# Kernel optimization log

Measured on AMD Instinct MI355X. Metric: run time of the kernel, lower is better.

## Reference

```python
import jax, jax.numpy as jnp
import numpy as np

B, S, E, H = 2, 2048, 768, 12
DK = E // H


def setup_inputs() -> dict:
    key = jax.random.key(0)
    ks = jax.random.split(key, 8)
    scale = 1.0 / np.sqrt(E)
    return {
        "key": jax.random.normal(ks[0], (B, S, E), jnp.float32),
        "query": jax.random.normal(ks[1], (B, S, E), jnp.float32),
        "value": jax.random.normal(ks[2], (B, S, E), jnp.float32),
        "mask": jax.random.randint(ks[3], (1, 1, S, S), 0, 2, jnp.int32),
        # nn.Linear params (w_k used for q/k/v as in the source; w_o output proj)
        "Wk": jax.random.uniform(ks[4], (E, E), jnp.float32, -scale, scale),
        "bk": jax.random.uniform(ks[5], (E,), jnp.float32, -scale, scale),
        "Wo": jax.random.uniform(ks[6], (E, E), jnp.float32, -scale, scale),
        "bo": jax.random.uniform(ks[7], (E,), jnp.float32, -scale, scale),
    }


def reference(key, query, value, mask, Wk, bk, Wo, bo):
    # NOTE: source module (faithfully) projects q, k, v all with w_k.
    k = (key @ Wk.T + bk).reshape(B, S, H, DK).transpose(0, 2, 1, 3)    # [B,H,S,DK]
    q = (query @ Wk.T + bk).reshape(B, S, H, DK).transpose(0, 2, 1, 3)
    v = (value @ Wk.T + bk).reshape(B, S, H, DK).transpose(0, 2, 1, 3)
    # quirk: scores MULTIPLIED by sqrt(d_k) (source bug, preserved)
    scores = jnp.einsum("bhsd,bhtd->bhst", q, k) * jnp.sqrt(jnp.float32(DK))
    # quirk: masked positions set to 1e-6 (not -inf), BEFORE softmax
    scores = jnp.where(mask == 0, jnp.float32(1e-6), scores)
    # dropout=0.0 -> identity (applied pre-softmax in source)
    attn = jax.nn.softmax(scores, axis=-1)                               # [B,H,S,S]
    x = jnp.einsum("bhst,bhtd->bhsd", attn, v)                           # [B,H,S,DK]
    x = x.transpose(0, 2, 1, 3).reshape(B, S, E)
    return x @ Wo.T + bo
```

## Files before the change

kernel.cpp:

```cpp
#include <hip/hip_runtime.h>

#define BB 2
#define SS 2048
#define EE 768
#define HH 12
#define DKK 64

typedef _Float16 h16;
typedef _Float16 half8 __attribute__((ext_vector_type(8)));
typedef _Float16 h16x4 __attribute__((ext_vector_type(4)));
typedef float f32x4 __attribute__((ext_vector_type(4)));

__global__ void pack_mask_k(const int* __restrict__ mask, unsigned* __restrict__ mp) {
    int idx = blockIdx.x * 256 + threadIdx.x;
    int base = idx * 32;
    const int4* m4 = (const int4*)(mask + base);
    unsigned w = 0;
#pragma unroll
    for (int i = 0; i < 8; ++i) {
        int4 v = m4[i];
        if (v.x) w |= 1u << (i * 4 + 0);
        if (v.y) w |= 1u << (i * 4 + 1);
        if (v.z) w |= 1u << (i * 4 + 2);
        if (v.w) w |= 1u << (i * 4 + 3);
    }
    mp[idx] = w;
}

__launch_bounds__(256)
__global__ void proj_gemm_k(const float* __restrict__ srcK, const float* __restrict__ srcQ,
                            const float* __restrict__ srcV, const float* __restrict__ Wk,
                            const float* __restrict__ bk,
                            h16* __restrict__ kh, h16* __restrict__ qh, h16* __restrict__ vtp) {
    __shared__ h16 As[64 * 64];
    __shared__ h16 Bs[128 * 64];
    const int bid = blockIdx.x;
    const int idx = (bid & 7) * 144 + (bid >> 3);
    const int z = idx / 384;
    const int rem = idx % 384;
    const int m0 = (rem / 6) * 64, n0 = (rem % 6) * 128;
    const float* src = (z == 0) ? srcK : ((z == 1) ? srcQ : srcV);
    const int tid = threadIdx.x, lane = tid & 63, wid = tid >> 6;
    const int l = lane & 15, gq = lane >> 4;
    f32x4 acc[4][2] = {};

    for (int k0 = 0; k0 < EE; k0 += 64) {
#pragma unroll
        for (int it = 0; it < 2; ++it) {
            int e8 = it * 256 + tid;
            int row = e8 >> 3, g = e8 & 7;
            const float* pa = src + (m0 + row) * EE + k0 + g * 8;
            float4 a0 = *(const float4*)pa, a1 = *(const float4*)(pa + 4);
            half8 ha = {(h16)a0.x, (h16)a0.y, (h16)a0.z, (h16)a0.w,
                        (h16)a1.x, (h16)a1.y, (h16)a1.z, (h16)a1.w};
            *(half8*)((char*)As + row * 128 + ((g ^ (row & 7)) << 4)) = ha;
        }
#pragma unroll
        for (int it = 0; it < 4; ++it) {
            int e8 = it * 256 + tid;
            int row = e8 >> 3, g = e8 & 7;
            const float* pb = Wk + (n0 + row) * EE + k0 + g * 8;
            float4 b0 = *(const float4*)pb, b1 = *(const float4*)(pb + 4);
            half8 hb = {(h16)b0.x, (h16)b0.y, (h16)b0.z, (h16)b0.w,
                        (h16)b1.x, (h16)b1.y, (h16)b1.z, (h16)b1.w};
            *(half8*)((char*)Bs + row * 128 + ((g ^ (row & 7)) << 4)) = hb;
        }
        __syncthreads();
#pragma unroll
        for (int ks = 0; ks < 2; ++ks) {
            half8 a[4], b[2];
#pragma unroll
            for (int rf = 0; rf < 4; ++rf) {
                int row = rf * 16 + l;
                int g = (ks * 4 + gq) ^ (row & 7);
                a[rf] = *(const half8*)((const char*)As + row * 128 + (g << 4));
            }
#pragma unroll
            for (int cf = 0; cf < 2; ++cf) {
                int row = wid * 32 + cf * 16 + l;
                int g = (ks * 4 + gq) ^ (row & 7);
                b[cf] = *(const half8*)((const char*)Bs + row * 128 + (g << 4));
            }
            __builtin_amdgcn_s_setprio(1);
#pragma unroll
            for (int rf = 0; rf < 4; ++rf)
#pragma unroll
                for (int cf = 0; cf < 2; ++cf)
                    acc[rf][cf] = __builtin_amdgcn_mfma_f32_16x16x32_f16(a[rf], b[cf], acc[rf][cf], 0, 0, 0);
            __builtin_amdgcn_s_setprio(0);
        }
        __syncthreads();
    }
    if (z == 2) {
#pragma unroll
        for (int rf = 0; rf < 4; ++rf)
#pragma unroll
            for (int cf = 0; cf < 2; ++cf) {
                int n = n0 + wid * 32 + cf * 16 + l;
                float bias = bk[n];
                int h = n >> 6, d = n & 63;
                int mb = m0 + rf * 16 + gq * 4;
                int b = mb >> 11, s = mb & 2047;
                h16x4 pv = {(h16)(acc[rf][cf][0] + bias), (h16)(acc[rf][cf][1] + bias),
                            (h16)(acc[rf][cf][2] + bias), (h16)(acc[rf][cf][3] + bias)};
                *(h16x4*)(vtp + ((long)((b * HH + h) * 64 + d)) * SS + s) = pv;
            }
    } else {
        h16* dst = (z == 0) ? kh : qh;
#pragma unroll
        for (int rf = 0; rf < 4; ++rf)
#pragma unroll
            for (int cf = 0; cf < 2; ++cf) {
                int n = n0 + wid * 32 + cf * 16 + l;
                float bias = bk[n];
                int h = n >> 6, d = n & 63;
#pragma unroll
                for (int j = 0; j < 4; ++j) {
                    int m = m0 + rf * 16 + gq * 4 + j;
                    int b = m >> 11, s = m & 2047;
                    dst[(((long)(b * HH + h) * SS + s) << 6) + d] = (h16)(acc[rf][cf][j] + bias);
                }
            }
    }
}

struct StageRegs { half8 k[2], v[2]; };

__device__ __forceinline__ void ld_stage(StageRegs& r, const h16* __restrict__ kg,
                                         const h16* __restrict__ vg,
                                         int kv0, int wid, int lane) {
    int rr = lane >> 3;
    int sg = (lane & 7) ^ rr;
#pragma unroll
    for (int i = 0; i < 2; ++i) {
        int row = wid * 16 + i * 8 + rr;
        r.k[i] = *(const half8*)(kg + (long)(kv0 + row) * DKK + sg * 8);
        r.v[i] = *(const half8*)(vg + (long)row * SS + kv0 + sg * 8);
    }
}

__device__ __forceinline__ void st_stage(h16* __restrict__ kl, h16* __restrict__ vl,
                                         const StageRegs& r, int wid, int lane) {
#pragma unroll
    for (int i = 0; i < 2; ++i) {
        *(half8*)(kl + wid * 1024 + i * 512 + lane * 8) = r.k[i];
        *(half8*)(vl + wid * 1024 + i * 512 + lane * 8) = r.v[i];
    }
}

__launch_bounds__(256, 3)
__global__ void attn_k(const h16* __restrict__ qh, const h16* __restrict__ kh,
                       const h16* __restrict__ vt, const unsigned long long* __restrict__ mp,
                       h16* __restrict__ xh) {
    __shared__ h16 Kbuf[2][4096];
    __shared__ h16 Vbuf[2][4096];
    __shared__ char Ps[8192];
    const int tid = threadIdx.x;
    const int lane = tid & 63, wid = tid >> 6;
    const int l = lane & 15, g = lane >> 4;
    const int bid = blockIdx.x;
    const int idx = (bid & 7) * 96 + (bid >> 3);
    const int q0 = (idx & 31) * 64 + wid * 16;
    const int bh = idx >> 5;
    const long base = (long)bh * SS * DKK;
    const h16* kg = kh + base;
    const h16* vg = vt + base;
    char* pbase = Ps + wid * 2048;

    half8 qf0, qf1;
    {
        const h16* qp = qh + base + (long)(q0 + l) * DKK + g * 8;
        qf0 = *(const half8*)qp;
        qf1 = *(const half8*)(qp + 32);
    }
    const unsigned long long* mrow = mp + (long)(q0 + l) * (SS / 64);

    f32x4 o[4] = {};
    float m2 = -INFINITY, lsum = 0.f;
    const float K2 = 8.0f * 1.44269504f;
    const float C2 = 1e-6f * 1.44269504f;

    StageRegs sr;
    ld_stage(sr, kg, vg, 0, wid, lane);
    st_stage(Kbuf[0], Vbuf[0], sr, wid, lane);
    __syncthreads();

    for (int t = 0; t < 32; ++t) {
        const h16* Kl = Kbuf[t & 1];
        const h16* Vl = Vbuf[t & 1];
        ld_stage(sr, kg, vg, ((t + 1) & 31) * 64, wid, lane);
        half8 ka[4], kb[4];
#pragma unroll
        for (int cf = 0; cf < 4; ++cf) {
            int row = cf * 16 + l;
            const h16* kp = Kl + row * 64;
            ka[cf] = *(const half8*)(kp + ((g ^ (row & 7)) << 3));
            kb[cf] = *(const half8*)(kp + (((4 + g) ^ (row & 7)) << 3));
        }
        f32x4 s[4];
        __builtin_amdgcn_s_setprio(1);
#pragma unroll
        for (int cf = 0; cf < 4; ++cf) {
            f32x4 z = {};
            z = __builtin_amdgcn_mfma_f32_16x16x32_f16(ka[cf], qf0, z, 0, 0, 0);
            z = __builtin_amdgcn_mfma_f32_16x16x32_f16(kb[cf], qf1, z, 0, 0, 0);
            s[cf] = z;
        }
        __builtin_amdgcn_s_setprio(0);
        unsigned long long mw = mrow[t];
        unsigned w0 = (unsigned)mw, w1 = (unsigned)(mw >> 32);
#pragma unroll
        for (int cf = 0; cf < 4; ++cf) {
            unsigned wcb = (cf & 2) ? w1 : w0;
#pragma unroll
            for (int j = 0; j < 4; ++j) {
                unsigned sh = ((cf & 1) << 4) + g * 4 + j;
                s[cf][j] = ((wcb >> sh) & 1u) ? s[cf][j] * K2 : C2;
            }
        }
        float pmax = fmaxf(fmaxf(s[0][0], s[0][1]), fmaxf(s[0][2], s[0][3]));
#pragma unroll
        for (int cf = 1; cf < 4; ++cf)
            pmax = fmaxf(pmax, fmaxf(fmaxf(s[cf][0], s[cf][1]), fmaxf(s[cf][2], s[cf][3])));
        if (!__all(pmax <= m2 + 11.0f)) {
            pmax = fmaxf(pmax, __shfl_xor(pmax, 16));
            pmax = fmaxf(pmax, __shfl_xor(pmax, 32));
            float mnew = fmaxf(m2, pmax);
            float alpha = __builtin_amdgcn_exp2f(m2 - mnew);
#pragma unroll
            for (int df = 0; df < 4; ++df)
#pragma unroll
                for (int j = 0; j < 4; ++j) o[df][j] *= alpha;
            lsum *= alpha;
            m2 = mnew;
        }
        float rs = 0.f;
#pragma unroll
        for (int cf = 0; cf < 4; ++cf)
#pragma unroll
            for (int j = 0; j < 4; ++j) {
                float p = __builtin_amdgcn_exp2f(s[cf][j] - m2);
                s[cf][j] = p;
                rs += p;
            }
        lsum += rs;
#pragma unroll
        for (int cf = 0; cf < 4; ++cf) {
            h16x4 pk = {(h16)s[cf][0], (h16)s[cf][1], (h16)s[cf][2], (h16)s[cf][3]};
            int gran = (2 * cf + (g >> 1)) ^ (l & 7);
            *(h16x4*)(pbase + l * 128 + gran * 16 + (g & 1) * 8) = pk;
        }
#pragma unroll
        for (int ks = 0; ks < 2; ++ks) {
            int gr = (ks * 4 + g) ^ (l & 7);
            half8 pf = *(const half8*)(pbase + l * 128 + gr * 16);
            half8 vk[4];
#pragma unroll
            for (int df = 0; df < 4; ++df) {
                int row = df * 16 + l;
                vk[df] = *(const half8*)(Vl + row * 64 + (((ks * 4 + g) ^ (row & 7)) << 3));
            }
            __builtin_amdgcn_s_setprio(1);
#pragma unroll
            for (int df = 0; df < 4; ++df)
                o[df] = __builtin_amdgcn_mfma_f32_16x16x32_f16(vk[df], pf, o[df], 0, 0, 0);
            __builtin_amdgcn_s_setprio(0);
        }
        st_stage(Kbuf[(t + 1) & 1], Vbuf[(t + 1) & 1], sr, wid, lane);
        __syncthreads();
    }

    lsum += __shfl_xor(lsum, 16);
    lsum += __shfl_xor(lsum, 32);
    float inv = 1.0f / lsum;
    int b = bh / HH, h = bh % HH;
    h16* xp = xh + (long)(b * SS + q0 + l) * EE + h * 64 + g * 4;
#pragma unroll
    for (int df = 0; df < 4; ++df) {
        h16x4 v4 = {(h16)(o[df][0] * inv), (h16)(o[df][1] * inv),
                    (h16)(o[df][2] * inv), (h16)(o[df][3] * inv)};
        *(h16x4*)(xp + df * 16) = v4;
    }
}

__launch_bounds__(256)
__global__ void out_gemm_k(const h16* __restrict__ xh, const float* __restrict__ Wo,
                           const float* __restrict__ bo, float* __restrict__ out) {
    __shared__ h16 As[64 * 64];
    __shared__ h16 Bs[64 * 64];
    const int bid = blockIdx.x;
    const int idx = (bid & 7) * 96 + (bid >> 3);
    const int m0 = (idx / 12) * 64, n0 = (idx % 12) * 64;
    const int tid = threadIdx.x, lane = tid & 63, wid = tid >> 6;
    const int l = lane & 15, gq = lane >> 4;
    const int wr = wid >> 1, wc = wid & 1;
    f32x4 acc[2][2] = {};

    for (int k0 = 0; k0 < EE; k0 += 64) {
#pragma unroll
        for (int it = 0; it < 2; ++it) {
            int e8 = it * 256 + tid;
            int row = e8 >> 3, g = e8 & 7;
            half8 ha = *(const half8*)(xh + (m0 + row) * EE + k0 + g * 8);
            const float* pb = Wo + (n0 + row) * EE + k0 + g * 8;
            float4 b0 = *(const float4*)pb, b1 = *(const float4*)(pb + 4);
            half8 hb = {(h16)b0.x, (h16)b0.y, (h16)b0.z, (h16)b0.w,
                        (h16)b1.x, (h16)b1.y, (h16)b1.z, (h16)b1.w};
            int sw = (g ^ (row & 7)) << 4;
            *(half8*)((char*)As + row * 128 + sw) = ha;
            *(half8*)((char*)Bs + row * 128 + sw) = hb;
        }
        __syncthreads();
#pragma unroll
        for (int ks = 0; ks < 2; ++ks) {
            half8 a[2], b[2];
#pragma unroll
            for (int rf = 0; rf < 2; ++rf) {
                int row = wr * 32 + rf * 16 + l;
                int g = (ks * 4 + gq) ^ (row & 7);
                a[rf] = *(const half8*)((const char*)As + row * 128 + (g << 4));
            }
#pragma unroll
            for (int cf = 0; cf < 2; ++cf) {
                int row = wc * 32 + cf * 16 + l;
                int g = (ks * 4 + gq) ^ (row & 7);
                b[cf] = *(const half8*)((const char*)Bs + row * 128 + (g << 4));
            }
            __builtin_amdgcn_s_setprio(1);
#pragma unroll
            for (int rf = 0; rf < 2; ++rf)
#pragma unroll
                for (int cf = 0; cf < 2; ++cf)
                    acc[rf][cf] = __builtin_amdgcn_mfma_f32_16x16x32_f16(a[rf], b[cf], acc[rf][cf], 0, 0, 0);
            __builtin_amdgcn_s_setprio(0);
        }
        __syncthreads();
    }
#pragma unroll
    for (int rf = 0; rf < 2; ++rf)
#pragma unroll
        for (int cf = 0; cf < 2; ++cf) {
            int n = n0 + wc * 32 + cf * 16 + l;
            float bias = bo[n];
#pragma unroll
            for (int j = 0; j < 4; ++j) {
                int m = m0 + wr * 32 + rf * 16 + gq * 4 + j;
                out[(long)m * EE + n] = acc[rf][cf][j] + bias;
            }
        }
}

extern "C" void kernel_launch(void* const* d_in, const int* in_sizes, int n_in,
                              void* d_out, int out_size, void* d_ws, size_t ws_size,
                              hipStream_t stream) {
    const float* key   = (const float*)d_in[0];
    const float* query = (const float*)d_in[1];
    const float* value = (const float*)d_in[2];
    const int*   mask  = (const int*)d_in[3];
    const float* Wk    = (const float*)d_in[4];
    const float* bk    = (const float*)d_in[5];
    const float* Wo    = (const float*)d_in[6];
    const float* bo    = (const float*)d_in[7];

    char* ws = (char*)d_ws;
    h16* qh = (h16*)(ws + 0);
    h16* kh = (h16*)(ws + 6291456);
    h16* vt = (h16*)(ws + 12582912);
    h16* xh = (h16*)(ws + 18874368);
    unsigned* mp = (unsigned*)(ws + 25165824);
    float* out = (float*)d_out;

    hipLaunchKernelGGL(pack_mask_k, dim3(SS * SS / 32 / 256), dim3(256), 0, stream, mask, mp);
    hipLaunchKernelGGL(proj_gemm_k, dim3(1152), dim3(256), 0, stream,
                       key, query, value, Wk, bk, kh, qh, vt);
    hipLaunchKernelGGL(attn_k, dim3(SS / 64 * BB * HH), dim3(256), 0, stream,
                       qh, kh, vt, (const unsigned long long*)mp, xh);
    hipLaunchKernelGGL(out_gemm_k, dim3(768), dim3(256), 0, stream, xh, Wo, bo, out);
}
```

Before: 138.7 us.

## Pre-convert inputs to fp16 and stage tiles via direct global-to-LDS loads

```diff
diff --git a/kernel.cpp b/kernel.cpp
--- a/kernel.cpp
+++ b/kernel.cpp
@@ -10,6 +10,12 @@
 typedef _Float16 half8 __attribute__((ext_vector_type(8)));
 typedef _Float16 h16x4 __attribute__((ext_vector_type(4)));
 typedef float f32x4 __attribute__((ext_vector_type(4)));
+
+__device__ __forceinline__ void gl_lds16(const void* g, void* l) {
+    __builtin_amdgcn_global_load_lds(
+        (const __attribute__((address_space(1))) unsigned int*)g,
+        (__attribute__((address_space(3))) unsigned int*)l, 16, 0, 0);
+}
 
 __global__ void pack_mask_k(const int* __restrict__ mask, unsigned* __restrict__ mp) {
     int idx = blockIdx.x * 256 + threadIdx.x;
@@ -27,9 +33,30 @@
     mp[idx] = w;
 }
 
+__global__ void cvt_k(const float* __restrict__ sK, const float* __restrict__ sQ,
+                      const float* __restrict__ sV, const float* __restrict__ sWk,
+                      const float* __restrict__ sWo,
+                      h16* __restrict__ dK, h16* __restrict__ dQ, h16* __restrict__ dV,
+                      h16* __restrict__ dWk, h16* __restrict__ dWo) {
+    long g = (long)blockIdx.x * 256 + threadIdx.x;
+    const float* src;
+    h16* dst;
+    long off;
+    if (g < 393216)        { src = sK;  dst = dK;  off = g; }
+    else if (g < 786432)   { src = sQ;  dst = dQ;  off = g - 393216; }
+    else if (g < 1179648)  { src = sV;  dst = dV;  off = g - 786432; }
+    else if (g < 1253376)  { src = sWk; dst = dWk; off = g - 1179648; }
+    else                   { src = sWo; dst = dWo; off = g - 1253376; }
+    const float* p = src + off * 8;
+    float4 a = *(const float4*)p, b = *(const float4*)(p + 4);
+    half8 h = {(h16)a.x, (h16)a.y, (h16)a.z, (h16)a.w,
+               (h16)b.x, (h16)b.y, (h16)b.z, (h16)b.w};
+    *(half8*)(dst + off * 8) = h;
+}
+
 __launch_bounds__(256)
-__global__ void proj_gemm_k(const float* __restrict__ srcK, const float* __restrict__ srcQ,
-                            const float* __restrict__ srcV, const float* __restrict__ Wk,
+__global__ void proj_gemm_k(const h16* __restrict__ keyh, const h16* __restrict__ qryh,
+                            const h16* __restrict__ valh, const h16* __restrict__ Wkh,
                             const float* __restrict__ bk,
                             h16* __restrict__ kh, h16* __restrict__ qh, h16* __restrict__ vtp) {
     __shared__ h16 As[64 * 64];
@@ -39,7 +66,7 @@
     const int z = idx / 384;
     const int rem = idx % 384;
     const int m0 = (rem / 6) * 64, n0 = (rem % 6) * 128;
-    const float* src = (z == 0) ? srcK : ((z == 1) ? srcQ : srcV);
+    const h16* src = (z == 0) ? keyh : ((z == 1) ? qryh : valh);
     const int tid = threadIdx.x, lane = tid & 63, wid = tid >> 6;
     const int l = lane & 15, gq = lane >> 4;
     f32x4 acc[4][2] = {};
@@ -47,23 +74,15 @@
     for (int k0 = 0; k0 < EE; k0 += 64) {
 #pragma unroll
         for (int it = 0; it < 2; ++it) {
-            int e8 = it * 256 + tid;
-            int row = e8 >> 3, g = e8 & 7;
-            const float* pa = src + (m0 + row) * EE + k0 + g * 8;
-            float4 a0 = *(const float4*)pa, a1 = *(const float4*)(pa + 4);
-            half8 ha = {(h16)a0.x, (h16)a0.y, (h16)a0.z, (h16)a0.w,
-                        (h16)a1.x, (h16)a1.y, (h16)a1.z, (h16)a1.w};
-            *(half8*)((char*)As + row * 128 + ((g ^ (row & 7)) << 4)) = ha;
+            int e = it * 256 + tid;
+            int row = e >> 3, slot = e & 7;
+            gl_lds16(src + (long)(m0 + row) * EE + k0 + ((slot ^ (row & 7)) << 3), As + e * 8);
         }
 #pragma unroll
         for (int it = 0; it < 4; ++it) {
-            int e8 = it * 256 + tid;
-            int row = e8 >> 3, g = e8 & 7;
-            const float* pb = Wk + (n0 + row) * EE + k0 + g * 8;
-            float4 b0 = *(const float4*)pb, b1 = *(const float4*)(pb + 4);
-            half8 hb = {(h16)b0.x, (h16)b0.y, (h16)b0.z, (h16)b0.w,
-                        (h16)b1.x, (h16)b1.y, (h16)b1.z, (h16)b1.w};
-            *(half8*)((char*)Bs + row * 128 + ((g ^ (row & 7)) << 4)) = hb;
+            int e = it * 256 + tid;
+            int row = e >> 3, slot = e & 7;
+            gl_lds16(Wkh + (long)(n0 + row) * EE + k0 + ((slot ^ (row & 7)) << 3), Bs + e * 8);
         }
         __syncthreads();
 #pragma unroll
@@ -121,30 +140,6 @@
                     dst[(((long)(b * HH + h) * SS + s) << 6) + d] = (h16)(acc[rf][cf][j] + bias);
                 }
             }
-    }
-}
-
-struct StageRegs { half8 k[2], v[2]; };
-
-__device__ __forceinline__ void ld_stage(StageRegs& r, const h16* __restrict__ kg,
-                                         const h16* __restrict__ vg,
-                                         int kv0, int wid, int lane) {
-    int rr = lane >> 3;
-    int sg = (lane & 7) ^ rr;
-#pragma unroll
-    for (int i = 0; i < 2; ++i) {
-        int row = wid * 16 + i * 8 + rr;
-        r.k[i] = *(const half8*)(kg + (long)(kv0 + row) * DKK + sg * 8);
-        r.v[i] = *(const half8*)(vg + (long)row * SS + kv0 + sg * 8);
-    }
-}
-
-__device__ __forceinline__ void st_stage(h16* __restrict__ kl, h16* __restrict__ vl,
-                                         const StageRegs& r, int wid, int lane) {
-#pragma unroll
-    for (int i = 0; i < 2; ++i) {
-        *(half8*)(kl + wid * 1024 + i * 512 + lane * 8) = r.k[i];
-        *(half8*)(vl + wid * 1024 + i * 512 + lane * 8) = r.v[i];
     }
 }
 
@@ -166,6 +161,7 @@
     const h16* kg = kh + base;
     const h16* vg = vt + base;
     char* pbase = Ps + wid * 2048;
+    const int rr = lane >> 3, sg = (lane & 7) ^ (lane >> 3);
 
     half8 qf0, qf1;
     {
@@ -180,15 +176,27 @@
     const float K2 = 8.0f * 1.44269504f;
     const float C2 = 1e-6f * 1.44269504f;
 
-    StageRegs sr;
-    ld_stage(sr, kg, vg, 0, wid, lane);
-    st_stage(Kbuf[0], Vbuf[0], sr, wid, lane);
+#pragma unroll
+    for (int i = 0; i < 2; ++i) {
+        int row = wid * 16 + i * 8 + rr;
+        gl_lds16(kg + (long)row * DKK + sg * 8, &Kbuf[0][wid * 1024 + i * 512 + lane * 8]);
+        gl_lds16(vg + (long)row * SS + sg * 8, &Vbuf[0][wid * 1024 + i * 512 + lane * 8]);
+    }
     __syncthreads();
 
     for (int t = 0; t < 32; ++t) {
         const h16* Kl = Kbuf[t & 1];
         const h16* Vl = Vbuf[t & 1];
-        ld_stage(sr, kg, vg, ((t + 1) & 31) * 64, wid, lane);
+        {
+            int kv0n = ((t + 1) & 31) * 64;
+            int nb = (t + 1) & 1;
+#pragma unroll
+            for (int i = 0; i < 2; ++i) {
+                int row = wid * 16 + i * 8 + rr;
+                gl_lds16(kg + (long)(kv0n + row) * DKK + sg * 8, &Kbuf[nb][wid * 1024 + i * 512 + lane * 8]);
+                gl_lds16(vg + (long)row * SS + kv0n + sg * 8, &Vbuf[nb][wid * 1024 + i * 512 + lane * 8]);
+            }
+        }
         half8 ka[4], kb[4];
 #pragma unroll
         for (int cf = 0; cf < 4; ++cf) {
@@ -266,7 +274,6 @@
                 o[df] = __builtin_amdgcn_mfma_f32_16x16x32_f16(vk[df], pf, o[df], 0, 0, 0);
             __builtin_amdgcn_s_setprio(0);
         }
-        st_stage(Kbuf[(t + 1) & 1], Vbuf[(t + 1) & 1], sr, wid, lane);
         __syncthreads();
     }
 
@@ -284,7 +291,7 @@
 }
 
 __launch_bounds__(256)
-__global__ void out_gemm_k(const h16* __restrict__ xh, const float* __restrict__ Wo,
+__global__ void out_gemm_k(const h16* __restrict__ xh, const h16* __restrict__ Woh,
                            const float* __restrict__ bo, float* __restrict__ out) {
     __shared__ h16 As[64 * 64];
     __shared__ h16 Bs[64 * 64];
@@ -299,16 +306,11 @@
     for (int k0 = 0; k0 < EE; k0 += 64) {
 #pragma unroll
         for (int it = 0; it < 2; ++it) {
-            int e8 = it * 256 + tid;
-            int row = e8 >> 3, g = e8 & 7;
-            half8 ha = *(const half8*)(xh + (m0 + row) * EE + k0 + g * 8);
-            const float* pb = Wo + (n0 + row) * EE + k0 + g * 8;
-            float4 b0 = *(const float4*)pb, b1 = *(const float4*)(pb + 4);
-            half8 hb = {(h16)b0.x, (h16)b0.y, (h16)b0.z, (h16)b0.w,
-                        (h16)b1.x, (h16)b1.y, (h16)b1.z, (h16)b1.w};
-            int sw = (g ^ (row & 7)) << 4;
-            *(half8*)((char*)As + row * 128 + sw) = ha;
-            *(half8*)((char*)Bs + row * 128 + sw) = hb;
+            int e = it * 256 + tid;
+            int row = e >> 3, slot = e & 7;
+            int gsl = (slot ^ (row & 7)) << 3;
+            gl_lds16(xh + (long)(m0 + row) * EE + k0 + gsl, As + e * 8);
+            gl_lds16(Woh + (long)(n0 + row) * EE + k0 + gsl, Bs + e * 8);
         }
         __syncthreads();
 #pragma unroll
@@ -363,17 +365,24 @@
     const float* bo    = (const float*)d_in[7];
 
     char* ws = (char*)d_ws;
-    h16* qh = (h16*)(ws + 0);
-    h16* kh = (h16*)(ws + 6291456);
-    h16* vt = (h16*)(ws + 12582912);
-    h16* xh = (h16*)(ws + 18874368);
-    unsigned* mp = (unsigned*)(ws + 25165824);
+    h16* keyh = (h16*)(ws + 0);
+    h16* qryh = (h16*)(ws + 6291456);
+    h16* valh = (h16*)(ws + 12582912);
+    h16* qh   = (h16*)(ws + 18874368);
+    h16* kh   = (h16*)(ws + 25165824);
+    h16* vt   = (h16*)(ws + 31457280);
+    h16* Wkh  = (h16*)(ws + 37748736);
+    h16* Woh  = (h16*)(ws + 38928384);
+    unsigned* mp = (unsigned*)(ws + 40108032);
+    h16* xh = keyh;
     float* out = (float*)d_out;
 
     hipLaunchKernelGGL(pack_mask_k, dim3(SS * SS / 32 / 256), dim3(256), 0, stream, mask, mp);
+    hipLaunchKernelGGL(cvt_k, dim3(5184), dim3(256), 0, stream,
+                       key, query, value, Wk, Wo, keyh, qryh, valh, Wkh, Woh);
     hipLaunchKernelGGL(proj_gemm_k, dim3(1152), dim3(256), 0, stream,
-                       key, query, value, Wk, bk, kh, qh, vt);
+                       keyh, qryh, valh, Wkh, bk, kh, qh, vt);
     hipLaunchKernelGGL(attn_k, dim3(SS / 64 * BB * HH), dim3(256), 0, stream,
                        qh, kh, vt, (const unsigned long long*)mp, xh);
-    hipLaunchKernelGGL(out_gemm_k, dim3(768), dim3(256), 0, stream, xh, Wo, bo, out);
-}
+    hipLaunchKernelGGL(out_gemm_k, dim3(768), dim3(256), 0, stream, xh, Woh, bo, out);
+}
```

Measured after the change: 117.1 us. 15.6% less time.
